# Kernel tuning notes

Hardware: AMD Instinct MI355X
Metric: run time of the kernel (lower is better)

The kernel has to match this reference:

```python
import jax, jax.numpy as jnp
import numpy as np

HEAD_DIM = 64

def setup_inputs() -> dict:
    key = jax.random.key(0)
    k1, k2, k3, k4 = jax.random.split(key, 4)
    B, S, D, H = 8, 2048, 1024, HEAD_DIM
    x = jax.random.normal(k1, (B, S, D), dtype=jnp.float32)
    scale = 1.0 / np.sqrt(D)
    W_q = jax.random.normal(k2, (H, D), dtype=jnp.float32) * scale
    W_k = jax.random.normal(k3, (H, D), dtype=jnp.float32) * scale
    W_v = jax.random.normal(k4, (H, D), dtype=jnp.float32) * scale
    return {"input_embeddings": x, "W_q": W_q, "W_k": W_k, "W_v": W_v}

def reference(input_embeddings, W_q, W_k, W_v):
    # Linear(model_dim, head_dim, bias=False): y = x @ W.T
    q = jnp.einsum('bsd,hd->bsh', input_embeddings, W_q)
    k = jnp.einsum('bsd,hd->bsh', input_embeddings, W_k)
    v = jnp.einsum('bsd,hd->bsh', input_embeddings, W_v)
    scores = jnp.einsum('bqh,bkh->bqk', q, k) / jnp.sqrt(jnp.float32(HEAD_DIM))
    S = scores.shape[-1]
    causal = jnp.tril(jnp.ones((S, S), dtype=bool))  # [S,S]
    scores = jnp.where(causal, scores, -jnp.inf)
    attn = jax.nn.softmax(scores, axis=-1)
    # dropout p=0.0 (eval-equivalent): identity
    return jnp.einsum('bqk,bkh->bqh', attn, v)
```

## Files before the change

### kernel.cpp

```cpp
#include <hip/hip_runtime.h>
#include <hip/hip_bf16.h>

typedef __bf16 bf16x8 __attribute__((ext_vector_type(8)));
typedef __bf16 bf16x4 __attribute__((ext_vector_type(4)));
typedef float  f32x4  __attribute__((ext_vector_type(4)));

#define NB  8
#define SEQ 2048
#define DM  1024
#define HD  64

#define WAITV4 asm volatile("s_waitcnt vmcnt(4)" ::: "memory")
#define WAITV0 asm volatile("s_waitcnt vmcnt(0)" ::: "memory")

__device__ __forceinline__ void gll16(const void* g, void* l) {
    __builtin_amdgcn_global_load_lds(
        (const __attribute__((address_space(1))) unsigned int*)g,
        (__attribute__((address_space(3))) unsigned int*)l, 16, 0, 0);
}

__global__ void k_convw(const float* __restrict__ Wq, const float* __restrict__ Wk,
                        const float* __restrict__ Wv, __bf16* __restrict__ Wb) {
    int idx = blockIdx.x * blockDim.x + threadIdx.x;
    int e = idx * 4;
    const float* src;
    if (e < 65536)       src = Wq + e;
    else if (e < 131072) src = Wk + (e - 65536);
    else                 src = Wv + (e - 131072);
    float4 v = *reinterpret_cast<const float4*>(src);
    bf16x4 o;
    o[0] = (__bf16)v.x; o[1] = (__bf16)v.y; o[2] = (__bf16)v.z; o[3] = (__bf16)v.w;
    *reinterpret_cast<bf16x4*>(Wb + e) = o;
}

__launch_bounds__(512, 4)
__global__ void k_proj(const float* __restrict__ X, const __bf16* __restrict__ Wb,
                       __bf16* __restrict__ Qb, __bf16* __restrict__ Kb,
                       __bf16* __restrict__ Vt) {
    __shared__ __align__(16) float  Xs[2][2048];
    __shared__ __align__(16) __bf16 Ws[2][12288];
    const int tid = threadIdx.x;
    const int w = tid >> 6, l = tid & 63;
    const int lr = l & 15, lg = l >> 4;
    const int wm = w >> 2, wn = w & 3;
    const int m0 = blockIdx.x * 32;

    const float* xsrc;
    {
        int u = w * 64 + l;
        int r_ = u >> 4, c_ = u & 15;
        xsrc = X + (size_t)(m0 + r_) * DM + (c_ ^ (r_ & 15)) * 4;
    }
    const __bf16* wsrc[3];
    #pragma unroll
    for (int j = 0; j < 3; ++j) {
        int u = w * 192 + j * 64 + l;
        int r_ = u >> 3, c_ = u & 7;
        wsrc[j] = Wb + (size_t)r_ * DM + (c_ ^ (r_ & 7)) * 8;
    }

    f32x4 acc[3];
    #pragma unroll
    for (int ct = 0; ct < 3; ++ct) acc[ct] = f32x4{0.f, 0.f, 0.f, 0.f};

    const int abase = (wm * 16 + lr) * 64;
    int bbase[3];
    #pragma unroll
    for (int ct = 0; ct < 3; ++ct) bbase[ct] = ((wn * 3 + ct) * 16 + lr) * 64;

    gll16(xsrc, &Xs[0][w * 256]);
    #pragma unroll
    for (int j = 0; j < 3; ++j) gll16(wsrc[j], &Ws[0][w * 1536 + j * 512]);

    #pragma unroll
    for (int t = 0; t < 16; ++t) {
        const int cur = t & 1;
        __builtin_amdgcn_s_barrier();
        if (t + 1 < 16) {
            gll16(xsrc + (size_t)(t + 1) * 64, &Xs[cur ^ 1][w * 256]);
            #pragma unroll
            for (int j = 0; j < 3; ++j)
                gll16(wsrc[j] + (size_t)(t + 1) * 64, &Ws[cur ^ 1][w * 1536 + j * 512]);
            WAITV4;
        } else {
            WAITV0;
        }
        const float*  Xp = &Xs[cur][0];
        const __bf16* Wp = &Ws[cur][0];
        #pragma unroll
        for (int ks = 0; ks < 2; ++ks) {
            f32x4 a0 = *reinterpret_cast<const f32x4*>(Xp + abase + ((ks * 8 + lg * 2)     ^ lr) * 4);
            f32x4 a1 = *reinterpret_cast<const f32x4*>(Xp + abase + ((ks * 8 + lg * 2 + 1) ^ lr) * 4);
            bf16x8 af;
            #pragma unroll
            for (int j = 0; j < 4; ++j) { af[j] = (__bf16)a0[j]; af[4 + j] = (__bf16)a1[j]; }
            #pragma unroll
            for (int ct = 0; ct < 3; ++ct) {
                bf16x8 bf = *reinterpret_cast<const bf16x8*>(
                    Wp + bbase[ct] + (((ks * 4 + lg) ^ (lr & 7)) * 8));
                acc[ct] = __builtin_amdgcn_mfma_f32_16x16x32_bf16(af, bf, acc[ct], 0, 0, 0);
            }
        }
    }

    const int rowbase = m0 + wm * 16 + lg * 4;
    #pragma unroll
    for (int ct = 0; ct < 3; ++ct) {
        const int ntile = wn * 3 + ct;
        const int mtx = ntile >> 2;
        const int d = (ntile & 3) * 16 + lr;
        if (mtx == 0) {
            #pragma unroll
            for (int r = 0; r < 4; ++r)
                Qb[(size_t)(rowbase + r) * HD + d] = (__bf16)(acc[ct][r] * 0.18033688f);
        } else if (mtx == 1) {
            #pragma unroll
            for (int r = 0; r < 4; ++r)
                Kb[(size_t)(rowbase + r) * HD + d] = (__bf16)acc[ct][r];
        } else {
            int bb = rowbase >> 11;
            int s0 = rowbase & 2047;
            bf16x4 vv;
            #pragma unroll
            for (int r = 0; r < 4; ++r) vv[r] = (__bf16)acc[ct][r];
            *reinterpret_cast<bf16x4*>(Vt + ((size_t)bb * HD + d) * SEQ + s0) = vv;
        }
    }
}

__launch_bounds__(512)
__global__ void k_attn(const __bf16* __restrict__ Qb, const __bf16* __restrict__ Kb,
                       const __bf16* __restrict__ Vt, __bf16* __restrict__ Opart,
                       float* __restrict__ ML, int T, int NC) {
    const int bid = blockIdx.x;
    const int b = bid / (16 * NC);
    const int rem = bid - b * 16 * NC;
    const int qt2 = rem / NC;
    const int c = rem - qt2 * NC;
    const int kmax = 2 * qt2 + 1;
    if (c * T > kmax) return;
    const int kt0 = c * T;
    const int nt = min(T, kmax + 1 - kt0);
    const int q0 = qt2 * 128;

    __shared__ __align__(16) __bf16 Ks[64][72];
    __shared__ __align__(16) __bf16 Vs[64][72];
    __shared__ __align__(16) __bf16 Ps[128][72];
    const int tid = threadIdx.x;
    const int w = tid >> 6, l = tid & 63;
    const int lr = l & 15, lg = l >> 4;
    const __bf16* Qp = Qb + (size_t)b * SEQ * HD;
    const __bf16* Kp = Kb + (size_t)b * SEQ * HD;
    const __bf16* Vp = Vt + (size_t)b * HD * SEQ;

    const int srow = tid >> 3, sc8 = (tid & 7) * 8;
    const int myq = q0 + 16 * w + lr;

    bf16x8 qa[2];
    #pragma unroll
    for (int ks = 0; ks < 2; ++ks)
        qa[ks] = *reinterpret_cast<const bf16x8*>(
            Qp + (size_t)myq * HD + ks * 32 + lg * 8);

    bf16x8 kpre, vpre;
    {
        const int k0 = kt0 * 64;
        kpre = *reinterpret_cast<const bf16x8*>(Kp + (size_t)(k0 + srow) * HD + sc8);
        vpre = *reinterpret_cast<const bf16x8*>(Vp + (size_t)srow * SEQ + k0 + sc8);
    }

    f32x4 oacc[4];
    #pragma unroll
    for (int r = 0; r < 4; ++r) oacc[r] = f32x4{0.f, 0.f, 0.f, 0.f};
    float m = -1e30f, lsum = 0.f;

    for (int it = 0; it < nt; ++it) {
        const int kt = kt0 + it;
        const int k0 = kt * 64;
        __syncthreads();
        *reinterpret_cast<bf16x8*>(&Ks[srow][sc8]) = kpre;
        *reinterpret_cast<bf16x8*>(&Vs[srow][sc8]) = vpre;
        __syncthreads();
        if (it + 1 < nt) {
            const int k0n = k0 + 64;
            kpre = *reinterpret_cast<const bf16x8*>(Kp + (size_t)(k0n + srow) * HD + sc8);
            vpre = *reinterpret_cast<const bf16x8*>(Vp + (size_t)srow * SEQ + k0n + sc8);
        }

        if (k0 > q0 + 16 * w + 15) continue;

        f32x4 sacc[4];
        #pragma unroll
        for (int t = 0; t < 4; ++t) sacc[t] = f32x4{0.f, 0.f, 0.f, 0.f};
        #pragma unroll
        for (int ks = 0; ks < 2; ++ks) {
            #pragma unroll
            for (int t = 0; t < 4; ++t) {
                bf16x8 kf = *reinterpret_cast<const bf16x8*>(&Ks[16 * t + lr][ks * 32 + lg * 8]);
                sacc[t] = __builtin_amdgcn_mfma_f32_16x16x32_bf16(kf, qa[ks], sacc[t], 0, 0, 0);
            }
        }

        float pmax = -1e30f;
        if (k0 + 63 > q0 + 16 * w) {
            #pragma unroll
            for (int t = 0; t < 4; ++t)
                #pragma unroll
                for (int r = 0; r < 4; ++r) {
                    float v = sacc[t][r];
                    if ((k0 + 16 * t + lg * 4 + r) > myq) v = -1e30f;
                    sacc[t][r] = v;
                    pmax = fmaxf(pmax, v);
                }
        } else {
            #pragma unroll
            for (int t = 0; t < 4; ++t)
                #pragma unroll
                for (int r = 0; r < 4; ++r) pmax = fmaxf(pmax, sacc[t][r]);
        }
        pmax = fmaxf(pmax, __shfl_xor(pmax, 16));
        pmax = fmaxf(pmax, __shfl_xor(pmax, 32));

        if (!__all(pmax <= m + 12.f)) {
            float mnew = fmaxf(m, pmax);
            float fsc = exp2f(m - mnew);
            m = mnew;
            lsum *= fsc;
            #pragma unroll
            for (int r = 0; r < 4; ++r) {
                float fq = __shfl(fsc, (l & 48) + lg * 4 + r);
                #pragma unroll
                for (int t2 = 0; t2 < 4; ++t2) oacc[t2][r] *= fq;
            }
        }

        float rs = 0.f;
        #pragma unroll
        for (int t = 0; t < 4; ++t)
            #pragma unroll
            for (int r = 0; r < 4; ++r) {
                float p = exp2f(sacc[t][r] - m);
                sacc[t][r] = p;
                rs += p;
            }
        rs += __shfl_xor(rs, 16);
        rs += __shfl_xor(rs, 32);
        lsum += rs;

        #pragma unroll
        for (int t = 0; t < 4; ++t) {
            bf16x4 pv;
            #pragma unroll
            for (int r = 0; r < 4; ++r) pv[r] = (__bf16)sacc[t][r];
            *reinterpret_cast<bf16x4*>(&Ps[16 * w + lr][16 * t + lg * 4]) = pv;
        }

        #pragma unroll
        for (int ks = 0; ks < 2; ++ks) {
            bf16x8 pa = *reinterpret_cast<const bf16x8*>(&Ps[16 * w + lr][ks * 32 + lg * 8]);
            #pragma unroll
            for (int t2 = 0; t2 < 4; ++t2) {
                bf16x8 vb = *reinterpret_cast<const bf16x8*>(&Vs[16 * t2 + lr][ks * 32 + lg * 8]);
                oacc[t2] = __builtin_amdgcn_mfma_f32_16x16x32_bf16(pa, vb, oacc[t2], 0, 0, 0);
            }
        }
    }

    const size_t slot = (size_t)bid;
    __bf16* op = Opart + slot * 8192;
    #pragma unroll
    for (int t2 = 0; t2 < 4; ++t2)
        #pragma unroll
        for (int r = 0; r < 4; ++r)
            op[(16 * w + lg * 4 + r) * 64 + 16 * t2 + lr] = (__bf16)oacc[t2][r];
    if (lg == 0) {
        float* ml = ML + slot * 256;
        int row = 16 * w + lr;
        ml[row * 2]     = m;
        ml[row * 2 + 1] = lsum;
    }
}

__launch_bounds__(512)
__global__ void k_merge(const __bf16* __restrict__ Opart, const float* __restrict__ ML,
                        float* __restrict__ Out, int T, int NC) {
    const int bq2 = blockIdx.x >> 1;
    const int half = blockIdx.x & 1;
    const int qt2 = bq2 & 15;
    const int nc = (2 * qt2 + 1) / T + 1;
    const int tid = threadIdx.x;
    const int row = tid >> 2;
    const int cg = (tid & 3) * 8 + half * 32;
    const int base = bq2 * NC;

    float M = -1e30f;
    for (int c = 0; c < nc; ++c)
        M = fmaxf(M, ML[(size_t)(base + c) * 256 + row * 2]);

    float L = 0.f;
    f32x4 a0{0,0,0,0}, a1{0,0,0,0};
    for (int c = 0; c < nc; ++c) {
        const float* ml = ML + (size_t)(base + c) * 256 + row * 2;
        float wgt = exp2f(ml[0] - M);
        L += ml[1] * wgt;
        bf16x8 v = *reinterpret_cast<const bf16x8*>(
            Opart + (size_t)(base + c) * 8192 + row * 64 + cg);
        #pragma unroll
        for (int j = 0; j < 4; ++j) {
            a0[j] += wgt * (float)v[j];
            a1[j] += wgt * (float)v[4 + j];
        }
    }
    float inv = 1.f / L;
    #pragma unroll
    for (int j = 0; j < 4; ++j) { a0[j] *= inv; a1[j] *= inv; }
    float* o = Out + ((size_t)bq2 * 128 + row) * 64 + cg;
    *reinterpret_cast<f32x4*>(o)     = a0;
    *reinterpret_cast<f32x4*>(o + 4) = a1;
}

extern "C" void kernel_launch(void* const* d_in, const int* in_sizes, int n_in,
                              void* d_out, int out_size, void* d_ws, size_t ws_size,
                              hipStream_t stream) {
    const float* x  = (const float*)d_in[0];
    const float* wq = (const float*)d_in[1];
    const float* wk = (const float*)d_in[2];
    const float* wv = (const float*)d_in[3];
    char* ws = (char*)d_ws;
    __bf16* Wb = (__bf16*)ws;
    __bf16* Qb = (__bf16*)(ws + 524288);
    __bf16* Kb = (__bf16*)(ws + 524288 + 2097152);
    __bf16* Vt = (__bf16*)(ws + 524288 + 2 * 2097152);
    const size_t base = 524288 + 3 * 2097152;
    float* out = (float*)d_out;

    int NC = (ws_size >= base + (size_t)(8 * 16 * 8) * 17408) ? 8 : 2;
    int T = 32 / NC;
    const int slots = 8 * 16 * NC;
    float*  ML    = (float*)(ws + base);
    __bf16* Opart = (__bf16*)(ws + base + (size_t)slots * 1024);

    hipLaunchKernelGGL(k_convw, dim3(192), dim3(256), 0, stream, wq, wk, wv, Wb);
    hipLaunchKernelGGL(k_proj,  dim3(512), dim3(512), 0, stream, x, Wb, Qb, Kb, Vt);
    hipLaunchKernelGGL(k_attn,  dim3(8 * 16 * NC), dim3(512), 0, stream,
                       Qb, Kb, Vt, Opart, ML, T, NC);
    hipLaunchKernelGGL(k_merge, dim3(256), dim3(512), 0, stream, Opart, ML, out, T, NC);
}
```

Baseline: 55.93 us.

## Double-buffer K/V tiles via direct global-to-LDS loads with XOR swizzle

Result: faster. 51.62 us (-7.7%).

```diff
diff --git a/kernel.cpp b/kernel.cpp
--- a/kernel.cpp
+++ b/kernel.cpp
@@ -143,8 +143,8 @@
     const int nt = min(T, kmax + 1 - kt0);
     const int q0 = qt2 * 128;
 
-    __shared__ __align__(16) __bf16 Ks[64][72];
-    __shared__ __align__(16) __bf16 Vs[64][72];
+    __shared__ __align__(16) __bf16 Ks[2][4096];
+    __shared__ __align__(16) __bf16 Vs[2][4096];
     __shared__ __align__(16) __bf16 Ps[128][72];
     const int tid = threadIdx.x;
     const int w = tid >> 6, l = tid & 63;
@@ -153,7 +153,10 @@
     const __bf16* Kp = Kb + (size_t)b * SEQ * HD;
     const __bf16* Vp = Vt + (size_t)b * HD * SEQ;
 
-    const int srow = tid >> 3, sc8 = (tid & 7) * 8;
+    const int srow = tid >> 3;
+    const int ssw  = ((l & 7) ^ (srow & 7)) * 8;
+    const __bf16* ksrc = Kp + (size_t)(kt0 * 64 + srow) * HD + ssw;
+    const __bf16* vsrc = Vp + (size_t)srow * SEQ + kt0 * 64 + ssw;
     const int myq = q0 + 16 * w + lr;
 
     bf16x8 qa[2];
@@ -162,29 +165,25 @@
         qa[ks] = *reinterpret_cast<const bf16x8*>(
             Qp + (size_t)myq * HD + ks * 32 + lg * 8);
 
-    bf16x8 kpre, vpre;
-    {
-        const int k0 = kt0 * 64;
-        kpre = *reinterpret_cast<const bf16x8*>(Kp + (size_t)(k0 + srow) * HD + sc8);
-        vpre = *reinterpret_cast<const bf16x8*>(Vp + (size_t)srow * SEQ + k0 + sc8);
-    }
-
     f32x4 oacc[4];
     #pragma unroll
     for (int r = 0; r < 4; ++r) oacc[r] = f32x4{0.f, 0.f, 0.f, 0.f};
     float m = -1e30f, lsum = 0.f;
+
+    gll16(ksrc, &Ks[0][w * 512]);
+    gll16(vsrc, &Vs[0][w * 512]);
 
     for (int it = 0; it < nt; ++it) {
         const int kt = kt0 + it;
         const int k0 = kt * 64;
-        __syncthreads();
-        *reinterpret_cast<bf16x8*>(&Ks[srow][sc8]) = kpre;
-        *reinterpret_cast<bf16x8*>(&Vs[srow][sc8]) = vpre;
-        __syncthreads();
+        const int cur = it & 1;
+        __builtin_amdgcn_s_barrier();
         if (it + 1 < nt) {
-            const int k0n = k0 + 64;
-            kpre = *reinterpret_cast<const bf16x8*>(Kp + (size_t)(k0n + srow) * HD + sc8);
-            vpre = *reinterpret_cast<const bf16x8*>(Vp + (size_t)srow * SEQ + k0n + sc8);
+            gll16(ksrc + (size_t)(it + 1) * 64 * HD, &Ks[cur ^ 1][w * 512]);
+            gll16(vsrc + (it + 1) * 64,              &Vs[cur ^ 1][w * 512]);
+            asm volatile("s_waitcnt vmcnt(2)" ::: "memory");
+        } else {
+            asm volatile("s_waitcnt vmcnt(0)" ::: "memory");
         }
 
         if (k0 > q0 + 16 * w + 15) continue;
@@ -196,7 +195,8 @@
         for (int ks = 0; ks < 2; ++ks) {
             #pragma unroll
             for (int t = 0; t < 4; ++t) {
-                bf16x8 kf = *reinterpret_cast<const bf16x8*>(&Ks[16 * t + lr][ks * 32 + lg * 8]);
+                bf16x8 kf = *reinterpret_cast<const bf16x8*>(
+                    &Ks[cur][(16 * t + lr) * 64 + (((ks * 4 + lg) ^ (lr & 7)) * 8)]);
                 sacc[t] = __builtin_amdgcn_mfma_f32_16x16x32_bf16(kf, qa[ks], sacc[t], 0, 0, 0);
             }
         }
@@ -260,7 +260,8 @@
             bf16x8 pa = *reinterpret_cast<const bf16x8*>(&Ps[16 * w + lr][ks * 32 + lg * 8]);
             #pragma unroll
             for (int t2 = 0; t2 < 4; ++t2) {
-                bf16x8 vb = *reinterpret_cast<const bf16x8*>(&Vs[16 * t2 + lr][ks * 32 + lg * 8]);
+                bf16x8 vb = *reinterpret_cast<const bf16x8*>(
+                    &Vs[cur][(16 * t2 + lr) * 64 + (((ks * 4 + lg) ^ (lr & 7)) * 8)]);
                 oacc[t2] = __builtin_amdgcn_mfma_f32_16x16x32_bf16(pa, vb, oacc[t2], 0, 0, 0);
             }
         }
@@ -334,7 +335,7 @@
     const size_t base = 524288 + 3 * 2097152;
     float* out = (float*)d_out;
 
-    int NC = (ws_size >= base + (size_t)(8 * 16 * 8) * 17408) ? 8 : 2;
+    int NC = (ws_size >= base + (size_t)(8 * 16 * 4) * 17408) ? 4 : 2;
     int T = 32 / NC;
     const int slots = 8 * 16 * NC;
     float*  ML    = (float*)(ws + base);
```
